# Kernel optimization log

Hardware: AMD Instinct MI355X
Metric: run time of the kernel (lower is better)

The kernel has to match this reference:

```python
import jax, jax.numpy as jnp
import numpy as np

# MiniCPM-style decode-step config (matches init_kwargs)
L, B, H, HKV, D, S, HID, FF = 8, 4, 16, 8, 64, 2048, 1024, 2816
SCALE_DEPTH = 1.4
ROPE_THETA = 10000.0
EPS = 1e-5


def _rms(x, w):
    v = jnp.mean(jnp.square(x), axis=-1, keepdims=True)
    return x * jax.lax.rsqrt(v + EPS) * w


def _rotate_half(x):
    x1, x2 = jnp.split(x, 2, axis=-1)
    return jnp.concatenate([-x2, x1], axis=-1)


def setup_inputs() -> dict:
    key = jax.random.key(0)
    ks = jax.random.split(key, 12)
    s = lambda i, shape, fan: jax.random.normal(ks[i], shape, jnp.float32) / np.sqrt(fan)
    return {
        "x": jax.random.normal(ks[0], (B, HID), jnp.float32),
        "k_cache": jax.random.normal(ks[1], (L, B, HKV, S, D), jnp.float32),
        "v_cache": jax.random.normal(ks[2], (L, B, HKV, S, D), jnp.float32),
        "Wq": s(3, (L, HID, H * D), HID),
        "Wk": s(4, (L, HID, HKV * D), HID),
        "Wv": s(5, (L, HID, HKV * D), HID),
        "Wo": s(6, (L, H * D, HID), H * D),
        "Wgate": s(7, (L, HID, FF), HID),
        "Wup": s(8, (L, HID, FF), HID),
        "Wdown": s(9, (L, FF, HID), FF),
        "norm1_w": jnp.ones((L, HID), jnp.float32),
        "norm2_w": jnp.ones((L, HID), jnp.float32),
        "final_norm_w": jnp.ones((HID,), jnp.float32),
        "current_length": 1500,
    }


def reference(x, k_cache, v_cache, Wq, Wk, Wv, Wo, Wgate, Wup, Wdown,
              norm1_w, norm2_w, final_norm_w, current_length):
    pos = jnp.asarray(current_length, jnp.int32)
    # RoPE for the single new position (rope_emb(position_id))
    inv_freq = 1.0 / (ROPE_THETA ** (jnp.arange(0, D, 2, dtype=jnp.float32) / D))
    ang = pos.astype(jnp.float32) * inv_freq            # [D/2]
    cos = jnp.concatenate([jnp.cos(ang), jnp.cos(ang)])  # [D]
    sin = jnp.concatenate([jnp.sin(ang), jnp.sin(ang)])
    positions = jnp.arange(S)
    write_mask = (positions == pos)[None, None, :, None]  # [1,1,S,1]
    valid = (positions <= pos)                            # [S]
    mup = SCALE_DEPTH / np.sqrt(L)
    g = H // HKV

    def layer(h, params):
        wq, wk, wv, wo, wg, wu, wd, n1, n2, kc, vc = params
        hn = _rms(h, n1)
        q = (hn @ wq).reshape(B, HKV, g, 1, D)   # grouped query heads
        k = (hn @ wk).reshape(B, HKV, 1, D)
        v = (hn @ wv).reshape(B, HKV, 1, D)
        q = q * cos + _rotate_half(q) * sin
        k = k * cos + _rotate_half(k) * sin
        # broadcast 'where' write into the full static cache (faithful to source)
        ak = jnp.where(write_mask, k, kc)         # [B,HKV,S,D]
        av = jnp.where(write_mask, v, vc)
        scores = jnp.einsum('bhgqd,bhsd->bhgqs', q, ak) / np.sqrt(D)
        scores = jnp.where(valid[None, None, None, None, :], scores, -jnp.inf)
        p = jax.nn.softmax(scores, axis=-1)
        o = jnp.einsum('bhgqs,bhsd->bhgqd', p, av).reshape(B, H * D)
        h = h + (o @ wo) * mup
        hn2 = _rms(h, n2)
        m = (jax.nn.silu(hn2 @ wg) * (hn2 @ wu)) @ wd
        h = h + m * mup
        return h, (k, v)  # one-position K/V updates [B,HKV,1,D]

    xs = (Wq, Wk, Wv, Wo, Wgate, Wup, Wdown, norm1_w, norm2_w, k_cache, v_cache)
    h, (k_upd, v_upd) = jax.lax.scan(layer, x, xs)
    h = _rms(h, final_norm_w)
    return h, k_upd, v_upd, pos + 1
```

## Files before the change

### kernel.cpp

```cpp
#include <hip/hip_runtime.h>

#define L_   8
#define B_   4
#define H_   16
#define HKV_ 8
#define D_   64
#define S_   2048
#define HID_ 1024
#define FF_  2816
#define EPS_ 1e-5f
#define MUP_ 0.49497474683058327f
#define SCALE_ 0.125f
#define NCH_ 32

#define OUT_H   0
#define OUT_K   4096
#define OUT_V   (4096 + 16384)
#define OUT_POS (4096 + 16384 + 16384)

enum {
  WS_HC  = 0,
  WS_QP  = 4096,
  WS_AM  = WS_QP + 262144,
  WS_AL  = WS_AM + 2048,
  WS_AO  = WS_AL + 2048,
  WS_GP  = WS_AO + 131072,
  WS_UP  = WS_GP + 360448,
  WS_END = WS_UP + 360448
};

__device__ __forceinline__ int read_pos_dev(const int* p) {
  int v = p[0];
  if (v >= 0 && v < S_) return v;
  float f = __int_as_float(v);
  if (f >= 0.0f && f <= (float)(S_ - 1)) return (int)(f + 0.5f);
  return 1500;
}

__device__ __forceinline__ float wave_sum(float v) {
  for (int m = 1; m < 64; m <<= 1) v += __shfl_xor(v, m);
  return v;
}
__device__ __forceinline__ float wave_max(float v) {
  for (int m = 1; m < 64; m <<= 1) v = fmaxf(v, __shfl_xor(v, m));
  return v;
}

__device__ __forceinline__ void rms_of(const float* hsrc, float* red, float* rs) {
  int t = threadIdx.x;
  float part[4] = {0.f, 0.f, 0.f, 0.f};
  #pragma unroll
  for (int j = 0; j < 4; ++j) {
    int c2 = t + j * 256;
    #pragma unroll
    for (int b = 0; b < 4; ++b) {
      float v = hsrc[b * HID_ + c2];
      part[b] += v * v;
    }
  }
  int w = t >> 6;
  #pragma unroll
  for (int b = 0; b < 4; ++b) {
    float s = wave_sum(part[b]);
    if ((t & 63) == 0) red[w * 4 + b] = s;
  }
  __syncthreads();
  #pragma unroll
  for (int b = 0; b < 4; ++b)
    rs[b] = rsqrtf((red[b] + red[4 + b] + red[8 + b] + red[12 + b]) * (1.0f / HID_) + EPS_);
}

__global__ void __launch_bounds__(256)
k1_qkv(const float* __restrict__ Wq, const float* __restrict__ Wk,
       const float* __restrict__ Wv, const float* __restrict__ n1,
       const float* __restrict__ x, float* __restrict__ ws, int l) {
  int cb = blockIdx.x & 7, kc = blockIdx.x >> 3;
  int t = threadIdx.x;
  int col = cb * 256 + t;
  const float* W; int wcol, stride;
  if (col < 1024)      { W = Wq + (size_t)l * HID_ * 1024; wcol = col;        stride = 1024; }
  else if (col < 1536) { W = Wk + (size_t)l * HID_ * 512;  wcol = col - 1024; stride = 512;  }
  else                 { W = Wv + (size_t)l * HID_ * 512;  wcol = col - 1536; stride = 512;  }
  const float* wp = W + (size_t)(kc * 32) * stride + wcol;
  float wv[32];
  #pragma unroll
  for (int i = 0; i < 32; ++i) wv[i] = wp[(size_t)i * stride];

  const float* hsrc = (l == 0) ? x : (ws + WS_HC);
  __shared__ float red[16];
  __shared__ __align__(16) float xs[4][32];
  float rs[4];
  rms_of(hsrc, red, rs);
  if (l == 0 && blockIdx.x < 4) {
    for (int j = 0; j < 4; ++j) {
      int c2 = t + j * 256;
      ws[WS_HC + blockIdx.x * HID_ + c2] = x[blockIdx.x * HID_ + c2];
    }
  }
  if (t < 128) {
    int b = t >> 5, i = t & 31;
    int gc = kc * 32 + i;
    xs[b][i] = hsrc[b * HID_ + gc] * rs[b] * n1[l * HID_ + gc];
  }
  __syncthreads();
  float a0 = 0.f, a1 = 0.f, a2 = 0.f, a3 = 0.f;
  #pragma unroll
  for (int i = 0; i < 32; ++i) {
    float w_ = wv[i];
    a0 += w_ * xs[0][i]; a1 += w_ * xs[1][i];
    a2 += w_ * xs[2][i]; a3 += w_ * xs[3][i];
  }
  ws[WS_QP + ((size_t)kc * 4 + 0) * 2048 + col] = a0;
  ws[WS_QP + ((size_t)kc * 4 + 1) * 2048 + col] = a1;
  ws[WS_QP + ((size_t)kc * 4 + 2) * 2048 + col] = a2;
  ws[WS_QP + ((size_t)kc * 4 + 3) * 2048 + col] = a3;
}

__global__ void __launch_bounds__(256)
k2_attn(const float* __restrict__ kcache, const float* __restrict__ vcache,
        const int* __restrict__ posp, float* __restrict__ ws,
        float* __restrict__ out, int l) {
  int bh = blockIdx.x >> 5, ns = blockIdx.x & 31;
  int b = bh >> 3, kv = bh & 7;
  int t = threadIdx.x;
  int w = t >> 6, lane = t & 63, r = lane >> 4, c = lane & 15;
  int pos = read_pos_dev(posp);
  __shared__ __align__(16) float Kst[64 * 68];
  __shared__ __align__(16) float Vst[64 * 68];
  __shared__ __align__(16) float qL[2][64];
  __shared__ __align__(16) float knL[64], vnL[64];
  __shared__ float rawL[256], sc0[64], sc1[64], red[8];
  __shared__ __align__(16) float oacc[2][4][64];

  const float* Kb = kcache + (((size_t)l * B_ + b) * HKV_ + kv) * S_ * 64;
  const float* Vb = vcache + (((size_t)l * B_ + b) * HKV_ + kv) * S_ * 64;
  int s0 = ns * 64;

  {
    const float4* Ksrc = (const float4*)(Kb + (size_t)s0 * 64);
    const float4* Vsrc = (const float4*)(Vb + (size_t)s0 * 64);
    #pragma unroll
    for (int i = 0; i < 4; ++i) {
      int f4 = t + i * 256;
      int row = f4 >> 4, c4 = f4 & 15;
      float4 kk = Ksrc[f4];
      float4 vv = Vsrc[f4];
      *(float4*)&Kst[row * 68 + 4 * c4] = kk;
      *(float4*)&Vst[row * 68 + 4 * c4] = vv;
    }
  }

  int cg;
  if (t < 128)      cg = (kv * 2 + (t >> 6)) * 64 + (t & 63);
  else if (t < 192) cg = 1024 + kv * 64 + (t & 63);
  else              cg = 1536 + kv * 64 + (t & 63);
  float s = 0.f;
  #pragma unroll
  for (int q = 0; q < 32; ++q) s += ws[WS_QP + ((size_t)q * 4 + b) * 2048 + cg];
  rawL[t] = s;
  __syncthreads();
  {
    int dd = t & 63;
    if (t < 192) {
      int idx = dd & 31;
      float inv = expf(-(float)idx * (1.0f / 32.0f) * 9.210340371976184f);
      float ang = (float)pos * inv;
      float sn, cs; __sincosf(ang, &sn, &cs);
      float partner = rawL[t ^ 32];
      float rot = (dd < 32) ? -partner : partner;
      float v = rawL[t] * cs + rot * sn;
      if (t < 128) qL[t >> 6][dd] = v;
      else {
        knL[dd] = v;
        if (ns == 0) out[OUT_K + (((size_t)l * B_ + b) * HKV_ + kv) * 64 + dd] = v;
      }
    } else {
      vnL[dd] = rawL[t];
      if (ns == 0) out[OUT_V + (((size_t)l * B_ + b) * HKV_ + kv) * 64 + dd] = rawL[t];
    }
  }
  __syncthreads();
  if (pos >= s0 && pos < s0 + 64) {
    int row = pos - s0;
    if (t < 64)                Kst[row * 68 + t] = knL[t];
    else if (t < 128)          Vst[row * 68 + (t - 64)] = vnL[t - 64];
  }
  __syncthreads();

  float4 q0 = *(float4*)&qL[0][4 * c];
  float4 q1 = *(float4*)&qL[1][4 * c];
  #pragma unroll
  for (int it = 0; it < 4; ++it) {
    int row = it * 16 + w * 4 + r;
    int sp = s0 + row;
    float4 k4 = *(float4*)&Kst[row * 68 + 4 * c];
    float d0 = k4.x * q0.x + k4.y * q0.y + k4.z * q0.z + k4.w * q0.w;
    float d1 = k4.x * q1.x + k4.y * q1.y + k4.z * q1.z + k4.w * q1.w;
    #pragma unroll
    for (int m = 1; m <= 8; m <<= 1) { d0 += __shfl_xor(d0, m); d1 += __shfl_xor(d1, m); }
    if (c == 0) {
      bool valid = (sp <= pos);
      sc0[row] = valid ? d0 * SCALE_ : -1e30f;
      sc1[row] = valid ? d1 * SCALE_ : -1e30f;
    }
  }
  __syncthreads();
  float v0 = (t < 64) ? sc0[t] : -1e30f;
  float v1 = (t < 64) ? sc1[t] : -1e30f;
  float m0 = wave_max(v0), m1 = wave_max(v1);
  if (lane == 0) { red[w] = m0; red[4 + w] = m1; }
  __syncthreads();
  m0 = fmaxf(fmaxf(red[0], red[1]), fmaxf(red[2], red[3]));
  m1 = fmaxf(fmaxf(red[4], red[5]), fmaxf(red[6], red[7]));
  float e0 = (t < 64) ? expf(v0 - m0) : 0.f;
  float e1 = (t < 64) ? expf(v1 - m1) : 0.f;
  __syncthreads();
  if (t < 64) { sc0[t] = e0; sc1[t] = e1; }
  float se0 = wave_sum(e0), se1 = wave_sum(e1);
  if (lane == 0) { red[w] = se0; red[4 + w] = se1; }
  __syncthreads();
  if (t == 0) {
    int base = ((b * HKV_ + kv) * 2) * NCH_ + ns;
    ws[WS_AM + base] = m0;          ws[WS_AM + base + NCH_] = m1;
    ws[WS_AL + base] = red[0] + red[1] + red[2] + red[3];
    ws[WS_AL + base + NCH_] = red[4] + red[5] + red[6] + red[7];
  }
  float4 a0 = make_float4(0.f, 0.f, 0.f, 0.f);
  float4 a1 = make_float4(0.f, 0.f, 0.f, 0.f);
  #pragma unroll
  for (int it = 0; it < 4; ++it) {
    int row = it * 16 + w * 4 + r;
    float4 v4 = *(float4*)&Vst[row * 68 + 4 * c];
    float p0 = sc0[row], p1 = sc1[row];
    a0.x += p0 * v4.x; a0.y += p0 * v4.y; a0.z += p0 * v4.z; a0.w += p0 * v4.w;
    a1.x += p1 * v4.x; a1.y += p1 * v4.y; a1.z += p1 * v4.z; a1.w += p1 * v4.w;
  }
  #pragma unroll
  for (int m = 16; m <= 32; m <<= 1) {
    a0.x += __shfl_xor(a0.x, m); a0.y += __shfl_xor(a0.y, m);
    a0.z += __shfl_xor(a0.z, m); a0.w += __shfl_xor(a0.w, m);
    a1.x += __shfl_xor(a1.x, m); a1.y += __shfl_xor(a1.y, m);
    a1.z += __shfl_xor(a1.z, m); a1.w += __shfl_xor(a1.w, m);
  }
  if (r == 0) {
    *(float4*)&oacc[0][w][4 * c] = a0;
    *(float4*)&oacc[1][w][4 * c] = a1;
  }
  __syncthreads();
  if (t < 64) {
    float r0 = oacc[0][0][t] + oacc[0][1][t] + oacc[0][2][t] + oacc[0][3][t];
    float r1 = oacc[1][0][t] + oacc[1][1][t] + oacc[1][2][t] + oacc[1][3][t];
    int h0 = kv * 2;
    ws[WS_AO + ((size_t)(b * H_ + h0)     * NCH_ + ns) * 64 + t] = r0;
    ws[WS_AO + ((size_t)(b * H_ + h0 + 1) * NCH_ + ns) * 64 + t] = r1;
  }
}

__global__ void __launch_bounds__(256)
k3_oproj(const float* __restrict__ Wo, float* __restrict__ ws, int l) {
  int cb = blockIdx.x & 3, kc = blockIdx.x >> 2;
  int t = threadIdx.x;
  int col = cb * 256 + t;
  const float* wp = Wo + ((size_t)l * HID_ + kc * 32) * HID_ + col;
  float wv[32];
  #pragma unroll
  for (int i = 0; i < 32; ++i) wv[i] = wp[(size_t)i * HID_];

  __shared__ __align__(16) float oT[32][4];
  if (t < 128) {
    int bb = t >> 5, jj = t & 31;
    int dim = kc * 32 + jj, h = dim >> 6, d = dim & 63;
    int mb = ((bb * HKV_ + (h >> 1)) * 2 + (h & 1)) * NCH_;
    float mx = -1e30f;
    #pragma unroll
    for (int n = 0; n < NCH_; ++n) mx = fmaxf(mx, ws[WS_AM + mb + n]);
    float ls = 0.f, os = 0.f;
    #pragma unroll
    for (int n = 0; n < NCH_; ++n) {
      float wg = expf(ws[WS_AM + mb + n] - mx);
      ls += wg * ws[WS_AL + mb + n];
      os += wg * ws[WS_AO + ((size_t)(bb * H_ + h) * NCH_ + n) * 64 + d];
    }
    oT[jj][bb] = os / ls;
  }
  __syncthreads();
  float a0 = 0.f, a1 = 0.f, a2 = 0.f, a3 = 0.f;
  #pragma unroll
  for (int i = 0; i < 32; ++i) {
    float w_ = wv[i];
    float4 o4 = *(float4*)&oT[i][0];
    a0 += w_ * o4.x; a1 += w_ * o4.y; a2 += w_ * o4.z; a3 += w_ * o4.w;
  }
  atomicAdd(ws + WS_HC + 0 * HID_ + col, MUP_ * a0);
  atomicAdd(ws + WS_HC + 1 * HID_ + col, MUP_ * a1);
  atomicAdd(ws + WS_HC + 2 * HID_ + col, MUP_ * a2);
  atomicAdd(ws + WS_HC + 3 * HID_ + col, MUP_ * a3);
}

__global__ void __launch_bounds__(256)
k4_gateup(const float* __restrict__ Wg, const float* __restrict__ Wu,
          const float* __restrict__ n2, float* __restrict__ ws, int l) {
  int cb = blockIdx.x % 11, kc = blockIdx.x / 11;
  int t = threadIdx.x;
  int col = cb * 256 + t;
  const float* wgp = Wg + ((size_t)l * HID_ + kc * 32) * FF_ + col;
  const float* wup = Wu + ((size_t)l * HID_ + kc * 32) * FF_ + col;
  float gv[32], uv[32];
  #pragma unroll
  for (int i = 0; i < 32; ++i) { gv[i] = wgp[(size_t)i * FF_]; uv[i] = wup[(size_t)i * FF_]; }

  const float* hsrc = ws + WS_HC;
  __shared__ float red[16];
  __shared__ __align__(16) float xs[4][32];
  float rs[4];
  rms_of(hsrc, red, rs);
  if (t < 128) {
    int b = t >> 5, i = t & 31;
    int gc = kc * 32 + i;
    xs[b][i] = hsrc[b * HID_ + gc] * rs[b] * n2[l * HID_ + gc];
  }
  __syncthreads();
  float g0 = 0.f, g1 = 0.f, g2 = 0.f, g3 = 0.f;
  float u0 = 0.f, u1 = 0.f, u2 = 0.f, u3 = 0.f;
  #pragma unroll
  for (int i = 0; i < 32; ++i) {
    float g = gv[i], u = uv[i];
    float x0 = xs[0][i], x1 = xs[1][i], x2 = xs[2][i], x3 = xs[3][i];
    g0 += g * x0; g1 += g * x1; g2 += g * x2; g3 += g * x3;
    u0 += u * x0; u1 += u * x1; u2 += u * x2; u3 += u * x3;
  }
  ws[WS_GP + ((size_t)kc * 4 + 0) * FF_ + col] = g0;
  ws[WS_GP + ((size_t)kc * 4 + 1) * FF_ + col] = g1;
  ws[WS_GP + ((size_t)kc * 4 + 2) * FF_ + col] = g2;
  ws[WS_GP + ((size_t)kc * 4 + 3) * FF_ + col] = g3;
  ws[WS_UP + ((size_t)kc * 4 + 0) * FF_ + col] = u0;
  ws[WS_UP + ((size_t)kc * 4 + 1) * FF_ + col] = u1;
  ws[WS_UP + ((size_t)kc * 4 + 2) * FF_ + col] = u2;
  ws[WS_UP + ((size_t)kc * 4 + 3) * FF_ + col] = u3;
}

__global__ void __launch_bounds__(256)
k5_down(const float* __restrict__ Wd, float* __restrict__ ws, int l) {
  int cb = blockIdx.x & 3, kc = blockIdx.x >> 2;
  int t = threadIdx.x;
  int col = cb * 256 + t;
  const float* wp = Wd + ((size_t)l * FF_ + kc * 64) * HID_ + col;
  float wv[64];
  #pragma unroll
  for (int i = 0; i < 64; ++i) wv[i] = wp[(size_t)i * HID_];

  __shared__ __align__(16) float mT[64][4];
  {
    int bb = t >> 6, jj = t & 63;
    int f = kc * 64 + jj;
    float g = 0.f, u = 0.f;
    #pragma unroll
    for (int k2 = 0; k2 < 32; ++k2) {
      g += ws[WS_GP + ((size_t)k2 * 4 + bb) * FF_ + f];
      u += ws[WS_UP + ((size_t)k2 * 4 + bb) * FF_ + f];
    }
    float sig = 1.f / (1.f + expf(-g));
    mT[jj][bb] = g * sig * u;
  }
  __syncthreads();
  float a0 = 0.f, a1 = 0.f, a2 = 0.f, a3 = 0.f;
  #pragma unroll
  for (int i = 0; i < 64; ++i) {
    float w_ = wv[i];
    float4 m4 = *(float4*)&mT[i][0];
    a0 += w_ * m4.x; a1 += w_ * m4.y; a2 += w_ * m4.z; a3 += w_ * m4.w;
  }
  atomicAdd(ws + WS_HC + 0 * HID_ + col, MUP_ * a0);
  atomicAdd(ws + WS_HC + 1 * HID_ + col, MUP_ * a1);
  atomicAdd(ws + WS_HC + 2 * HID_ + col, MUP_ * a2);
  atomicAdd(ws + WS_HC + 3 * HID_ + col, MUP_ * a3);
}

__global__ void __launch_bounds__(256)
k6_final(const float* __restrict__ fw, const int* __restrict__ posp,
         float* __restrict__ ws, float* __restrict__ out) {
  int b = blockIdx.x, t = threadIdx.x;
  __shared__ float red[4];
  float hv[4];
  float part = 0.f;
  for (int j = 0; j < 4; ++j) {
    float v = ws[WS_HC + b * HID_ + t + j * 256];
    hv[j] = v; part += v * v;
  }
  part = wave_sum(part);
  if ((t & 63) == 0) red[t >> 6] = part;
  __syncthreads();
  float rs = rsqrtf((red[0] + red[1] + red[2] + red[3]) * (1.0f / HID_) + EPS_);
  for (int j = 0; j < 4; ++j) {
    int c2 = t + j * 256;
    out[OUT_H + b * HID_ + c2] = hv[j] * rs * fw[c2];
  }
  if (b == 0 && t == 0) out[OUT_POS] = (float)(read_pos_dev(posp) + 1);
}

extern "C" void kernel_launch(void* const* d_in, const int* in_sizes, int n_in,
                              void* d_out, int out_size, void* d_ws, size_t ws_size,
                              hipStream_t stream) {
  const float* x   = (const float*)d_in[0];
  const float* kcp = (const float*)d_in[1];
  const float* vcp = (const float*)d_in[2];
  const float* Wq  = (const float*)d_in[3];
  const float* Wk  = (const float*)d_in[4];
  const float* Wv  = (const float*)d_in[5];
  const float* Wo  = (const float*)d_in[6];
  const float* Wg  = (const float*)d_in[7];
  const float* Wu  = (const float*)d_in[8];
  const float* Wd  = (const float*)d_in[9];
  const float* n1  = (const float*)d_in[10];
  const float* n2  = (const float*)d_in[11];
  const float* fw  = (const float*)d_in[12];
  const int*   pos = (const int*)d_in[13];
  float* ws  = (float*)d_ws;
  float* out = (float*)d_out;

  for (int l = 0; l < L_; ++l) {
    k1_qkv   <<< 256, 256, 0, stream>>>(Wq, Wk, Wv, n1, x, ws, l);
    k2_attn  <<<1024, 256, 0, stream>>>(kcp, vcp, pos, ws, out, l);
    k3_oproj <<< 128, 256, 0, stream>>>(Wo, ws, l);
    k4_gateup<<< 352, 256, 0, stream>>>(Wg, Wu, n2, ws, l);
    k5_down  <<< 176, 256, 0, stream>>>(Wd, ws, l);
  }
  k6_final<<<4, 256, 0, stream>>>(fw, pos, ws, out);
}
```

Baseline: 316.9 us.

## Skip fully-masked KV chunks and read K/V directly from global memory

```diff
diff --git a/kernel.cpp b/kernel.cpp
--- a/kernel.cpp
+++ b/kernel.cpp
@@ -125,8 +125,15 @@
   int t = threadIdx.x;
   int w = t >> 6, lane = t & 63, r = lane >> 4, c = lane & 15;
   int pos = read_pos_dev(posp);
-  __shared__ __align__(16) float Kst[64 * 68];
-  __shared__ __align__(16) float Vst[64 * 68];
+  int s0 = ns * 64;
+  if (s0 > pos) {
+    if (t == 0) {
+      int base = ((b * HKV_ + kv) * 2) * NCH_ + ns;
+      ws[WS_AM + base] = -1e30f;       ws[WS_AM + base + NCH_] = -1e30f;
+      ws[WS_AL + base] = 0.f;          ws[WS_AL + base + NCH_] = 0.f;
+    }
+    return;
+  }
   __shared__ __align__(16) float qL[2][64];
   __shared__ __align__(16) float knL[64], vnL[64];
   __shared__ float rawL[256], sc0[64], sc1[64], red[8];
@@ -134,21 +141,6 @@
 
   const float* Kb = kcache + (((size_t)l * B_ + b) * HKV_ + kv) * S_ * 64;
   const float* Vb = vcache + (((size_t)l * B_ + b) * HKV_ + kv) * S_ * 64;
-  int s0 = ns * 64;
-
-  {
-    const float4* Ksrc = (const float4*)(Kb + (size_t)s0 * 64);
-    const float4* Vsrc = (const float4*)(Vb + (size_t)s0 * 64);
-    #pragma unroll
-    for (int i = 0; i < 4; ++i) {
-      int f4 = t + i * 256;
-      int row = f4 >> 4, c4 = f4 & 15;
-      float4 kk = Ksrc[f4];
-      float4 vv = Vsrc[f4];
-      *(float4*)&Kst[row * 68 + 4 * c4] = kk;
-      *(float4*)&Vst[row * 68 + 4 * c4] = vv;
-    }
-  }
 
   int cg;
   if (t < 128)      cg = (kv * 2 + (t >> 6)) * 64 + (t & 63);
@@ -180,12 +172,6 @@
     }
   }
   __syncthreads();
-  if (pos >= s0 && pos < s0 + 64) {
-    int row = pos - s0;
-    if (t < 64)                Kst[row * 68 + t] = knL[t];
-    else if (t < 128)          Vst[row * 68 + (t - 64)] = vnL[t - 64];
-  }
-  __syncthreads();
 
   float4 q0 = *(float4*)&qL[0][4 * c];
   float4 q1 = *(float4*)&qL[1][4 * c];
@@ -193,7 +179,8 @@
   for (int it = 0; it < 4; ++it) {
     int row = it * 16 + w * 4 + r;
     int sp = s0 + row;
-    float4 k4 = *(float4*)&Kst[row * 68 + 4 * c];
+    float4 k4 = (sp == pos) ? *(float4*)&knL[4 * c]
+                            : *(const float4*)&Kb[(size_t)sp * 64 + 4 * c];
     float d0 = k4.x * q0.x + k4.y * q0.y + k4.z * q0.z + k4.w * q0.w;
     float d1 = k4.x * q1.x + k4.y * q1.y + k4.z * q1.z + k4.w * q1.w;
     #pragma unroll
@@ -230,7 +217,9 @@
   #pragma unroll
   for (int it = 0; it < 4; ++it) {
     int row = it * 16 + w * 4 + r;
-    float4 v4 = *(float4*)&Vst[row * 68 + 4 * c];
+    int sp = s0 + row;
+    float4 v4 = (sp == pos) ? *(float4*)&vnL[4 * c]
+                            : *(const float4*)&Vb[(size_t)sp * 64 + 4 * c];
     float p0 = sc0[row], p1 = sc1[row];
     a0.x += p0 * v4.x; a0.y += p0 * v4.y; a0.z += p0 * v4.z; a0.w += p0 * v4.w;
     a1.x += p1 * v4.x; a1.y += p1 * v4.y; a1.z += p1 * v4.z; a1.w += p1 * v4.w;
```

Measured after the change: 300.4 us. -5.2%, faster.
